# Kernel tuning notes

Hardware: AMD Instinct MI355X
Metric: run time of the kernel (lower is better)

The kernel has to match this reference:

```python
import jax, jax.numpy as jnp
import numpy as np

B, T, OMNI_D, STATIC_D = 128, 1024, 32, 16
H = 64            # hidden // 2 (per-direction GRU size)
HID = 128         # hidden
PHYS_LEN, N_PHYS = 432, 5


def _gelu(x):
    return jax.nn.gelu(x, approximate=False)  # torch GELU default = exact erf


def _ln(x, g, b, eps=1e-5):
    m = jnp.mean(x, -1, keepdims=True)
    v = jnp.var(x, -1, keepdims=True)
    return (x - m) / jnp.sqrt(v + eps) * g + b


def _gru_layer(x, Wih, Whh, bih, bhh, reverse):
    # PyTorch GRU cell math; x: [B,T,D] -> (outputs [B,T,H], h_final [B,H])
    Hh = Whh.shape[1]
    gi = jnp.einsum('btd,gd->btg', x, Wih) + bih  # precompute input projections
    if reverse:
        gi = gi[:, ::-1]
    gi = jnp.swapaxes(gi, 0, 1)  # [T,B,3H]
    h0 = jnp.zeros((x.shape[0], Hh), x.dtype)

    def step(h, g):
        gh = h @ Whh.T + bhh
        r = jax.nn.sigmoid(g[:, :Hh] + gh[:, :Hh])
        z = jax.nn.sigmoid(g[:, Hh:2 * Hh] + gh[:, Hh:2 * Hh])
        n = jnp.tanh(g[:, 2 * Hh:] + r * gh[:, 2 * Hh:])
        hn = (1 - z) * n + z * h
        return hn, hn

    hT, ys = jax.lax.scan(step, h0, gi)
    ys = jnp.swapaxes(ys, 0, 1)
    if reverse:
        ys = ys[:, ::-1]
    return ys, hT


def _conv1d(x, W, b, pad, dil):
    y = jax.lax.conv_general_dilated(x, W, (1,), [(pad, pad)], rhs_dilation=(dil,),
                                     dimension_numbers=('NCH', 'OIH', 'NCH'))
    return y + b[None, :, None]


def setup_inputs():
    key = jax.random.key(0)
    ks = iter(jax.random.split(key, 64))

    def rn(shape, s=0.05):
        return jax.random.normal(next(ks), shape, jnp.float32) * s

    inp = {
        'omni_seq': rn((B, T, OMNI_D), 1.0),
        'static_x': rn((B, STATIC_D), 1.0),
        'phys': rn((B, N_PHYS, PHYS_LEN), 1.0),
    }
    for l, d_in in (('l0', OMNI_D), ('l1', 2 * H)):
        for dr in ('f', 'b'):
            inp[f'gru_Wih_{l}{dr}'] = rn((3 * H, d_in))
            inp[f'gru_Whh_{l}{dr}'] = rn((3 * H, H))
            inp[f'gru_bih_{l}{dr}'] = rn((3 * H,))
            inp[f'gru_bhh_{l}{dr}'] = rn((3 * H,))
    inp['sm_W'] = rn((H, STATIC_D)); inp['sm_b'] = rn((H,))
    inp['sm_ln_g'] = jnp.ones((H,), jnp.float32); inp['sm_ln_b'] = jnp.zeros((H,), jnp.float32)
    inp['gate_W'] = rn((N_PHYS, H)); inp['gate_b'] = rn((N_PHYS,))
    inp['attn_in_W'] = rn((3 * N_PHYS, N_PHYS)); inp['attn_in_b'] = rn((3 * N_PHYS,))
    inp['attn_out_W'] = rn((N_PHYS, N_PHYS)); inp['attn_out_b'] = rn((N_PHYS,))
    for i, ksz in ((1, 3), (2, 5), (3, 9)):
        inp[f'conv{i}_W'] = rn((HID // 4, N_PHYS, ksz)); inp[f'conv{i}_b'] = rn((HID // 4,))
    FUSED = HID + H + 3 * (HID // 4)  # 288
    inp['head_ln_g'] = jnp.ones((FUSED,), jnp.float32); inp['head_ln_b'] = jnp.zeros((FUSED,), jnp.float32)
    inp['head_W1'] = rn((HID, FUSED)); inp['head_b1'] = rn((HID,))
    inp['head_W2'] = rn((PHYS_LEN, HID)); inp['head_b2'] = rn((PHYS_LEN,))
    return inp


def reference(omni_seq, static_x, phys,
              gru_Wih_l0f, gru_Whh_l0f, gru_bih_l0f, gru_bhh_l0f,
              gru_Wih_l0b, gru_Whh_l0b, gru_bih_l0b, gru_bhh_l0b,
              gru_Wih_l1f, gru_Whh_l1f, gru_bih_l1f, gru_bhh_l1f,
              gru_Wih_l1b, gru_Whh_l1b, gru_bih_l1b, gru_bhh_l1b,
              sm_W, sm_b, sm_ln_g, sm_ln_b, gate_W, gate_b,
              attn_in_W, attn_in_b, attn_out_W, attn_out_b,
              conv1_W, conv1_b, conv2_W, conv2_b, conv3_W, conv3_b,
              head_ln_g, head_ln_b, head_W1, head_b1, head_W2, head_b2):
    # --- bidirectional 2-layer GRU (eval mode: dropout off) ---
    y0f, _ = _gru_layer(omni_seq, gru_Wih_l0f, gru_Whh_l0f, gru_bih_l0f, gru_bhh_l0f, False)
    y0b, _ = _gru_layer(omni_seq, gru_Wih_l0b, gru_Whh_l0b, gru_bih_l0b, gru_bhh_l0b, True)
    x1 = jnp.concatenate([y0f, y0b], -1)
    _, hf = _gru_layer(x1, gru_Wih_l1f, gru_Whh_l1f, gru_bih_l1f, gru_bhh_l1f, False)
    _, hb = _gru_layer(x1, gru_Wih_l1b, gru_Whh_l1b, gru_bih_l1b, gru_bhh_l1b, True)
    omni_embed = jnp.concatenate([hf, hb], -1)  # h_omni[-2] ++ h_omni[-1], [B,128]
    # --- static MLP ---
    static_embed = _ln(_gelu(static_x @ sm_W.T + sm_b), sm_ln_g, sm_ln_b)  # [B,64]
    # --- gating on phys channels ---
    gates = jax.nn.sigmoid(static_embed @ gate_W.T + gate_b)[..., None]  # [B,5,1]
    p = phys * gates  # [B,5,432]
    # --- tiny MHA: embed_dim=5, 5 heads, head_dim=1 -> scale = 1/sqrt(1) = 1 ---
    pt = jnp.swapaxes(p, 1, 2)  # [B,432,5]
    qkv = pt @ attn_in_W.T + attn_in_b
    E = N_PHYS
    q, k, v = qkv[..., :E], qkv[..., E:2 * E], qkv[..., 2 * E:]
    scores = jnp.einsum('bih,bjh->bhij', q, k)  # [B,5,432,432]
    attn = jax.nn.softmax(scores, -1)
    ao = jnp.einsum('bhij,bjh->bih', attn, v)
    ao = ao @ attn_out_W.T + attn_out_b  # out_proj
    p = jnp.swapaxes(ao, 1, 2)  # [B,5,432]
    # --- dilated conv branches + GELU + adaptive avg pool (= mean over length) ---
    c1 = _gelu(_conv1d(p, conv1_W, conv1_b, 1, 1)).mean(-1)
    c2 = _gelu(_conv1d(p, conv2_W, conv2_b, 2, 2)).mean(-1)
    c3 = _gelu(_conv1d(p, conv3_W, conv3_b, 4, 4)).mean(-1)
    fused = jnp.concatenate([omni_embed, static_embed, c1, c2, c3], 1)  # [B,288]
    h = _ln(fused, head_ln_g, head_ln_b)
    h = _gelu(h @ head_W1.T + head_b1)  # dropout off in eval
    return h @ head_W2.T + head_b2  # [B,432]
```

## Files before the change

### kernel.cpp

```cpp
#include <hip/hip_runtime.h>
#include <stdint.h>

#define B_ 128
#define T_ 1024
#define BT_ (B_*T_)
#define H_ 64
#define G_ 192
#define PL_ 432
#define NP_ 5
#define FUSED_ 288
#define N_IN 41

typedef unsigned short u16;
typedef __attribute__((ext_vector_type(8))) short bf16x8;
typedef __attribute__((ext_vector_type(4))) float f32x4;
typedef _Float16 h2 __attribute__((ext_vector_type(2)));
typedef _Float16 h8 __attribute__((ext_vector_type(8)));

__device__ inline float bf2f(u16 u){ union{float f; unsigned int i;} c; c.i = ((unsigned int)u)<<16; return c.f; }
__device__ inline u16 f2bf(float f){ unsigned int u = __float_as_uint(f); unsigned int r = (u + 0x7fffu + ((u>>16)&1u))>>16; return (u16)r; }
__device__ inline _Float16 bf2h(u16 u){ return (_Float16)bf2f(u); }
__device__ inline float sigm(float x){ return 1.f/(1.f+__expf(-x)); }
__device__ inline float tanh_(float x){ float t = __expf(fminf(fmaxf(2.f*x,-30.f),30.f)); return (t-1.f)/(t+1.f); }
__device__ inline float gelu_(float x){ return 0.5f*x*(1.f + erff(x*0.70710678118654752f)); }
__device__ inline float wredsum(float v){
  #pragma unroll
  for(int o=32;o>0;o>>=1) v += __shfl_xor(v,o);
  return v;
}

#if __has_builtin(__builtin_amdgcn_fdot2)
__device__ inline float dot2(h2 a, h2 b, float c){ return __builtin_amdgcn_fdot2(a, b, c, false); }
#else
__device__ inline float dot2(h2 a, h2 b, float c){ return c + (float)a.x*(float)b.x + (float)a.y*(float)b.y; }
#endif

struct CvtArgs {
  const void* src[N_IN];
  unsigned dstOff[N_IN];
  unsigned cnt[N_IN];
  unsigned blkStart[N_IN+1];
};

__global__ __launch_bounds__(256) void convert_k(CvtArgs a, u16* __restrict__ dst){
  const bool isbf = (((const u16*)a.src[21])[0] == 0x3F80u);
  int b = blockIdx.x;
  int lo = 0, hi = N_IN;
  while (hi - lo > 1){ int mid = (lo+hi)>>1; if (a.blkStart[mid] <= (unsigned)b) lo = mid; else hi = mid; }
  const int i = lo;
  const unsigned lb = (unsigned)b - a.blkStart[i];
  const unsigned n = a.cnt[i];
  u16* d = dst + a.dstOff[i];
  if (isbf){
    const u16* s = (const u16*)a.src[i];
    #pragma unroll
    for(int e=0;e<8;e++){ unsigned idx = lb*2048u + e*256u + threadIdx.x; if (idx < n) d[idx] = s[idx]; }
  } else {
    const float* s = (const float*)a.src[i];
    #pragma unroll
    for(int e=0;e<8;e++){ unsigned idx = lb*2048u + e*256u + threadIdx.x; if (idx < n) d[idx] = f2bf(s[idx]); }
  }
}

template<int K>
__global__ __launch_bounds__(256) void gi_gemm(const u16* __restrict__ A,
    const u16* __restrict__ Wf, const u16* __restrict__ Wb,
    const u16* __restrict__ biasF, const u16* __restrict__ biasB,
    u16* __restrict__ out)
{
  const int wv = threadIdx.x >> 6, lane = threadIdx.x & 63;
  const int l15 = lane & 15, quad = lane >> 4;
  const size_t mBase = (size_t)blockIdx.x*64 + wv*16;

  bf16x8 afr[K/32];
  #pragma unroll
  for(int kc=0;kc<K/32;kc++)
    afr[kc] = *(const bf16x8*)(A + (mBase + l15)*K + kc*32 + quad*8);

  #pragma unroll
  for(int half=0; half<2; ++half){
    const u16* W    = half ? Wb : Wf;
    const u16* bias = half ? biasB : biasF;
    u16* o = out + (size_t)half * BT_ * G_;
    for(int nt=0; nt<12; ++nt){
      int n = nt*16 + l15;
      f32x4 acc = {0.f,0.f,0.f,0.f};
      #pragma unroll
      for(int kc=0;kc<K/32;kc++){
        bf16x8 bfr = *(const bf16x8*)(W + n*K + kc*32 + quad*8);
        acc = __builtin_amdgcn_mfma_f32_16x16x32_bf16(afr[kc], bfr, acc, 0,0,0);
      }
      float bv = bf2f(bias[n]);
      #pragma unroll
      for(int r=0;r<4;r++){
        size_t row = mBase + quad*4 + r;
        o[row*G_ + n] = f2bf(acc[r] + bv);
      }
    }
  }
}

__global__ __launch_bounds__(64)
void recur(const u16* __restrict__ gi,
    const u16* __restrict__ WhF, const u16* __restrict__ WhB,
    const u16* __restrict__ bhF, const u16* __restrict__ bhB,
    u16* __restrict__ y_x1, float* __restrict__ hfin, int layer)
{
  const int chain = blockIdx.x;
  const int dir = chain >> 7;
  const int b = chain & 127;
  const int j = threadIdx.x;
  const u16* Wh = dir ? WhB : WhF;
  const u16* bh = dir ? bhB : bhF;

  h2 wr[32], wz[32], wn[32];
  #pragma unroll
  for(int k8=0;k8<8;k8++){
    uint4 q;
    q = *(const uint4*)(Wh + (size_t)j*64 + k8*8);
    wr[4*k8+0] = (h2){bf2h((u16)(q.x&0xffffu)), bf2h((u16)(q.x>>16))};
    wr[4*k8+1] = (h2){bf2h((u16)(q.y&0xffffu)), bf2h((u16)(q.y>>16))};
    wr[4*k8+2] = (h2){bf2h((u16)(q.z&0xffffu)), bf2h((u16)(q.z>>16))};
    wr[4*k8+3] = (h2){bf2h((u16)(q.w&0xffffu)), bf2h((u16)(q.w>>16))};
    q = *(const uint4*)(Wh + (size_t)(64+j)*64 + k8*8);
    wz[4*k8+0] = (h2){bf2h((u16)(q.x&0xffffu)), bf2h((u16)(q.x>>16))};
    wz[4*k8+1] = (h2){bf2h((u16)(q.y&0xffffu)), bf2h((u16)(q.y>>16))};
    wz[4*k8+2] = (h2){bf2h((u16)(q.z&0xffffu)), bf2h((u16)(q.z>>16))};
    wz[4*k8+3] = (h2){bf2h((u16)(q.w&0xffffu)), bf2h((u16)(q.w>>16))};
    q = *(const uint4*)(Wh + (size_t)(128+j)*64 + k8*8);
    wn[4*k8+0] = (h2){bf2h((u16)(q.x&0xffffu)), bf2h((u16)(q.x>>16))};
    wn[4*k8+1] = (h2){bf2h((u16)(q.y&0xffffu)), bf2h((u16)(q.y>>16))};
    wn[4*k8+2] = (h2){bf2h((u16)(q.z&0xffffu)), bf2h((u16)(q.z>>16))};
    wn[4*k8+3] = (h2){bf2h((u16)(q.w&0xffffu)), bf2h((u16)(q.w>>16))};
  }
  const float bhr = bf2f(bh[j]), bhz = bf2f(bh[64+j]), bhn = bf2f(bh[128+j]);

  __shared__ __align__(16) u16 giLds[2][3072];
  __shared__ _Float16 hSf[64];
  h8* hS8 = (h8*)hSf;
  hSf[j] = (_Float16)0.f;

  const u16* giC = gi + (size_t)chain * T_ * G_;

  auto issue_chunk = [&](int c, int buf){
    int tbase = dir ? (1008 - c*16) : (c*16);
    const u16* src = giC + (size_t)tbase*G_ + j*8;
    u16* dst = &giLds[buf][0];
    #pragma unroll
    for(int i=0;i<6;i++){
      __builtin_amdgcn_global_load_lds(
        (const __attribute__((address_space(1))) void*)(src + i*512),
        (__attribute__((address_space(3))) void*)(dst + i*512), 16, 0, 0);
    }
  };

  issue_chunk(0, 0);

  float h = 0.f;
  for(int c=0; c<64; ++c){
    asm volatile("s_waitcnt vmcnt(0)" ::: "memory");
    if (c < 63) issue_chunk(c+1, (c+1)&1);
    const u16* gbuf = &giLds[c&1][0];
    #pragma unroll 2
    for(int ls=0; ls<16; ++ls){
      int row = dir ? (15-ls) : ls;
      const u16* rowp = gbuf + row*G_;
      float r0=bhr, r1=0.f, z0=bhz, z1=0.f, n0=bhn, n1=0.f;
      #pragma unroll
      for(int k=0;k<8;k++){
        h8 hv = hS8[k];
        h2 p0 = __builtin_shufflevector(hv, hv, 0, 1);
        h2 p1 = __builtin_shufflevector(hv, hv, 2, 3);
        h2 p2 = __builtin_shufflevector(hv, hv, 4, 5);
        h2 p3 = __builtin_shufflevector(hv, hv, 6, 7);
        r0 = dot2(wr[4*k+0], p0, r0); r1 = dot2(wr[4*k+1], p1, r1);
        r0 = dot2(wr[4*k+2], p2, r0); r1 = dot2(wr[4*k+3], p3, r1);
        z0 = dot2(wz[4*k+0], p0, z0); z1 = dot2(wz[4*k+1], p1, z1);
        z0 = dot2(wz[4*k+2], p2, z0); z1 = dot2(wz[4*k+3], p3, z1);
        n0 = dot2(wn[4*k+0], p0, n0); n1 = dot2(wn[4*k+1], p1, n1);
        n0 = dot2(wn[4*k+2], p2, n0); n1 = dot2(wn[4*k+3], p3, n1);
      }
      float gr = bf2f(rowp[j]), gz = bf2f(rowp[64+j]), gn = bf2f(rowp[128+j]);

      float r  = sigm(gr + (r0+r1));
      float z  = sigm(gz + (z0+z1));
      float nn = tanh_(gn + r*(n0+n1));
      h = (1.f - z)*nn + z*h;

      hSf[j] = (_Float16)h;

      if (layer == 0){
        int s = c*16 + ls;
        int t = dir ? (T_-1-s) : s;
        y_x1[((size_t)b*T_ + t)*128 + dir*64 + j] = f2bf(h);
      }
    }
  }
  if (layer == 1) hfin[b*FUSED_ + dir*64 + j] = h;
}

__global__ __launch_bounds__(64) void static_k(const u16* __restrict__ sx,
   const u16* __restrict__ smW, const u16* __restrict__ smb,
   const u16* __restrict__ lng, const u16* __restrict__ lnb,
   const u16* __restrict__ gW, const u16* __restrict__ gb,
   float* __restrict__ fused, float* __restrict__ gates)
{
  int b = blockIdx.x, j = threadIdx.x;
  float xr[16];
  #pragma unroll
  for(int k=0;k<16;k++) xr[k] = bf2f(sx[b*16+k]);
  float acc = bf2f(smb[j]);
  #pragma unroll
  for(int k=0;k<16;k++) acc += xr[k]*bf2f(smW[j*16+k]);
  float xg = gelu_(acc);
  float m = wredsum(xg)*(1.f/64.f);
  float d = xg - m;
  float v = wredsum(d*d)*(1.f/64.f);
  float se = d*rsqrtf(v+1e-5f)*bf2f(lng[j]) + bf2f(lnb[j]);
  fused[b*FUSED_ + 128 + j] = se;
  #pragma unroll
  for(int i=0;i<5;i++){
    float p = se*bf2f(gW[i*64+j]);
    float s = wredsum(p);
    if (j == 0) gates[b*5+i] = sigm(s + bf2f(gb[i]));
  }
}

__global__ __launch_bounds__(448) void qkv_k(const u16* __restrict__ phys,
   const float* __restrict__ gates, const u16* __restrict__ aW,
   const u16* __restrict__ ab, float* __restrict__ qkv)
{
  int b = blockIdx.x, l = threadIdx.x;
  if (l >= PL_) return;
  float pv[5];
  #pragma unroll
  for(int i=0;i<5;i++) pv[i] = bf2f(phys[((size_t)b*5+i)*PL_ + l]) * gates[b*5+i];
  #pragma unroll
  for(int c=0;c<15;c++){
    float a = bf2f(ab[c]);
    #pragma unroll
    for(int i=0;i<5;i++) a += pv[i]*bf2f(aW[c*5+i]);
    qkv[((size_t)b*15+c)*PL_ + l] = a;
  }
}

__global__ __launch_bounds__(256) void attn_k(const float* __restrict__ qkv,
                                              float* __restrict__ ao)
{
  int h = blockIdx.x, b = blockIdx.y;
  int tid = threadIdx.x;
  __shared__ float kS[PL_], vS[PL_];
  __shared__ float red[32];
  const float* qb = qkv + ((size_t)b*15 + h)*PL_;
  const float* kb = qkv + ((size_t)b*15 + 5 + h)*PL_;
  const float* vb = qkv + ((size_t)b*15 + 10 + h)*PL_;
  for(int j=tid;j<PL_;j+=256){ kS[j]=kb[j]; vS[j]=vb[j]; }
  __syncthreads();
  float lmax=-1e30f, lmin=1e30f;
  for(int j=tid;j<PL_;j+=256){ float kv=kS[j]; lmax=fmaxf(lmax,kv); lmin=fminf(lmin,kv); }
  #pragma unroll
  for(int o=32;o>0;o>>=1){ lmax=fmaxf(lmax,__shfl_xor(lmax,o)); lmin=fminf(lmin,__shfl_xor(lmin,o)); }
  int wv = tid>>6;
  if ((tid&63)==0){ red[wv]=lmax; red[8+wv]=lmin; }
  __syncthreads();
  if (tid==0){
    float mx=red[0], mn=red[8];
    for(int i=1;i<4;i++){ mx=fmaxf(mx,red[i]); mn=fminf(mn,red[8+i]); }
    red[16]=mx; red[17]=mn;
  }
  __syncthreads();
  float kmx=red[16], kmn=red[17];
  for(int i=tid;i<PL_;i+=256){
    float s = qb[i];
    float m = fmaxf(s*kmx, s*kmn);
    float den=0.f, num=0.f;
    #pragma unroll 4
    for(int j=0;j<PL_;j++){
      float e = __expf(s*kS[j]-m);
      den += e; num += e*vS[j];
    }
    ao[((size_t)b*PL_+i)*5 + h] = num/den;
  }
}

__global__ __launch_bounds__(448) void proj_k(const float* __restrict__ ao,
   const u16* __restrict__ oW, const u16* __restrict__ ob, float* __restrict__ p2)
{
  int b = blockIdx.x, l = threadIdx.x;
  if (l >= PL_) return;
  float a[5];
  #pragma unroll
  for(int hh=0;hh<5;hh++) a[hh] = ao[((size_t)b*PL_+l)*5 + hh];
  #pragma unroll
  for(int c=0;c<5;c++){
    float s = bf2f(ob[c]);
    #pragma unroll
    for(int hh=0;hh<5;hh++) s += a[hh]*bf2f(oW[c*5+hh]);
    p2[((size_t)b*5+c)*PL_ + l] = s;
  }
}

template<int KS, int DIL, int PAD>
__device__ inline void do_conv(const float* pS, const u16* Wc, const u16* bc,
                               float* fused, int b, int o, int p, int cslot)
{
  const int Lout = PL_ + 2*PAD - DIL*(KS-1);
  float w[5][KS];
  #pragma unroll
  for(int i=0;i<5;i++)
    #pragma unroll
    for(int t=0;t<KS;t++) w[i][t] = bf2f(Wc[(o*5+i)*KS + t]);
  float bias = bf2f(bc[o]);
  float acc = 0.f;
  for(int l=p; l<Lout; l+=8){
    float s = bias;
    #pragma unroll
    for(int t=0;t<KS;t++){
      int idx = l - PAD + t*DIL;
      if (idx >= 0 && idx < PL_){
        #pragma unroll
        for(int i=0;i<5;i++) s += w[i][t]*pS[i*PL_ + idx];
      }
    }
    acc += gelu_(s);
  }
  #pragma unroll
  for(int off=1;off<8;off<<=1) acc += __shfl_xor(acc,off);
  if (p == 0) fused[b*FUSED_ + 192 + cslot*32 + o] = acc/(float)Lout;
}

__global__ __launch_bounds__(256) void conv_k(const float* __restrict__ p2,
  const u16* __restrict__ W1c, const u16* __restrict__ b1c,
  const u16* __restrict__ W2c, const u16* __restrict__ b2c,
  const u16* __restrict__ W3c, const u16* __restrict__ b3c,
  float* __restrict__ fused)
{
  int b = blockIdx.x;
  __shared__ float pS[5*PL_];
  for(int idx=threadIdx.x; idx<5*PL_; idx+=256) pS[idx] = p2[(size_t)b*5*PL_ + idx];
  __syncthreads();
  int o = threadIdx.x >> 3, p = threadIdx.x & 7;
  do_conv<3,1,1>(pS, W1c, b1c, fused, b, o, p, 0);
  do_conv<5,2,2>(pS, W2c, b2c, fused, b, o, p, 1);
  do_conv<9,4,4>(pS, W3c, b3c, fused, b, o, p, 2);
}

__global__ __launch_bounds__(448) void head_k(const float* __restrict__ fused,
   const u16* __restrict__ lng, const u16* __restrict__ lnb,
   const u16* __restrict__ W1, const u16* __restrict__ b1,
   const u16* __restrict__ W2, const u16* __restrict__ b2,
   void* __restrict__ out, const u16* __restrict__ detect)
{
  const bool isbf = (detect[0] == 0x3F80u);
  int b = blockIdx.x, tid = threadIdx.x;
  __shared__ float fS[FUSED_];
  __shared__ float hS[128];
  __shared__ float red[32];
  float v = (tid < FUSED_) ? fused[b*FUSED_ + tid] : 0.f;
  float s1 = wredsum(v);
  float s2 = wredsum(v*v);
  int wv = tid>>6;
  if ((tid&63)==0){ red[wv]=s1; red[8+wv]=s2; }
  __syncthreads();
  if (tid==0){
    float S=0.f, SS=0.f;
    for(int i=0;i<7;i++){ S+=red[i]; SS+=red[8+i]; }
    float m = S/288.f;
    red[16]=m; red[17]=SS/288.f - m*m;
  }
  __syncthreads();
  float m = red[16], var = red[17];
  if (tid < FUSED_) fS[tid] = (v-m)*rsqrtf(var+1e-5f)*bf2f(lng[tid]) + bf2f(lnb[tid]);
  __syncthreads();
  if (tid < 128){
    float a = bf2f(b1[tid]);
    const u16* wr = W1 + (size_t)tid*FUSED_;
    #pragma unroll
    for(int k8=0;k8<36;k8++){
      uint4 q = *(const uint4*)(wr + k8*8);
      a += fS[8*k8+0]*bf2f((u16)(q.x&0xffffu)) + fS[8*k8+1]*bf2f((u16)(q.x>>16))
         + fS[8*k8+2]*bf2f((u16)(q.y&0xffffu)) + fS[8*k8+3]*bf2f((u16)(q.y>>16))
         + fS[8*k8+4]*bf2f((u16)(q.z&0xffffu)) + fS[8*k8+5]*bf2f((u16)(q.z>>16))
         + fS[8*k8+6]*bf2f((u16)(q.w&0xffffu)) + fS[8*k8+7]*bf2f((u16)(q.w>>16));
    }
    hS[tid] = gelu_(a);
  }
  __syncthreads();
  if (tid < PL_){
    float a = bf2f(b2[tid]);
    const u16* wr = W2 + (size_t)tid*128;
    #pragma unroll
    for(int k8=0;k8<16;k8++){
      uint4 q = *(const uint4*)(wr + k8*8);
      a += hS[8*k8+0]*bf2f((u16)(q.x&0xffffu)) + hS[8*k8+1]*bf2f((u16)(q.x>>16))
         + hS[8*k8+2]*bf2f((u16)(q.y&0xffffu)) + hS[8*k8+3]*bf2f((u16)(q.y>>16))
         + hS[8*k8+4]*bf2f((u16)(q.z&0xffffu)) + hS[8*k8+5]*bf2f((u16)(q.z>>16))
         + hS[8*k8+6]*bf2f((u16)(q.w&0xffffu)) + hS[8*k8+7]*bf2f((u16)(q.w>>16));
    }
    size_t oi = (size_t)b*PL_ + tid;
    if (isbf) ((u16*)out)[oi] = f2bf(a);
    else      ((float*)out)[oi] = a;
  }
}

extern "C" void kernel_launch(void* const* d_in, const int* in_sizes, int n_in,
                              void* d_out, int out_size, void* d_ws, size_t ws_size,
                              hipStream_t stream)
{
  static const unsigned cnts[N_IN] = {
    4194304, 2048, 276480,
    6144, 12288, 192, 192,
    6144, 12288, 192, 192,
    24576, 12288, 192, 192,
    24576, 12288, 192, 192,
    1024, 64, 64, 64,
    320, 5,
    75, 15,
    25, 5,
    480, 32, 800, 32, 1440, 32,
    288, 288,
    36864, 128, 55296, 432
  };

  char* ws = (char*)d_ws;
  size_t off = 0;
  auto alloc = [&](size_t bytes){ size_t o = off; off = (off + bytes + 255) & ~(size_t)255; return o; };

  CvtArgs ca;
  const u16* cin[N_IN];
  unsigned totalBlocks = 0;
  for (int i=0;i<N_IN;i++){
    ca.src[i] = d_in[i];
    ca.cnt[i] = cnts[i];
    size_t o = alloc((size_t)cnts[i]*2);
    ca.dstOff[i] = (unsigned)(o/2);
    cin[i] = (const u16*)(ws + o);
    ca.blkStart[i] = totalBlocks;
    totalBlocks += (cnts[i] + 2047u)/2048u;
  }
  ca.blkStart[N_IN] = totalBlocks;
  u16* canon = (u16*)ws;

  u16*   gi    = (u16*)  (ws + alloc((size_t)2*BT_*G_*2));
  u16*   x1    = (u16*)  (ws + alloc((size_t)BT_*128*2));
  float* fused = (float*)(ws + alloc((size_t)B_*FUSED_*4));
  float* gates = (float*)(ws + alloc((size_t)B_*5*4));
  float* qkv   = (float*)(ws + alloc((size_t)B_*15*PL_*4));
  float* ao    = (float*)(ws + alloc((size_t)B_*PL_*5*4));
  float* p2    = (float*)(ws + alloc((size_t)B_*5*PL_*4));
  (void)ws_size; (void)in_sizes; (void)n_in; (void)out_size;

  convert_k<<<totalBlocks, 256, 0, stream>>>(ca, canon);

  gi_gemm<32><<<BT_/64, 256, 0, stream>>>(cin[0], cin[3], cin[7], cin[5], cin[9], gi);
  recur<<<256, 64, 0, stream>>>(gi, cin[4], cin[8], cin[6], cin[10], x1, nullptr, 0);
  gi_gemm<128><<<BT_/64, 256, 0, stream>>>(x1, cin[11], cin[15], cin[13], cin[17], gi);
  recur<<<256, 64, 0, stream>>>(gi, cin[12], cin[16], cin[14], cin[18], nullptr, fused, 1);
  static_k<<<128, 64, 0, stream>>>(cin[1], cin[19], cin[20], cin[21], cin[22], cin[23], cin[24], fused, gates);
  qkv_k<<<128, 448, 0, stream>>>(cin[2], gates, cin[25], cin[26], qkv);
  attn_k<<<dim3(5,128), 256, 0, stream>>>(qkv, ao);
  proj_k<<<128, 448, 0, stream>>>(ao, cin[27], cin[28], p2);
  conv_k<<<128, 256, 0, stream>>>(p2, cin[29], cin[30], cin[31], cin[32], cin[33], cin[34], fused);
  head_k<<<128, 448, 0, stream>>>(fused, cin[35], cin[36], cin[37], cin[38], cin[39], cin[40],
                                  d_out, (const u16*)d_in[21]);
}
```

Before: 1.288 ms.

## Split GRU recurrence gates across three waves with a dedicated loader wave

The recurrence kernel grows from one wave to four per chain. Three waves each compute one gate's hidden-state dot products, exchanging pre-activations through LDS with a workgroup barrier every timestep. The fourth wave prefetches gi chunks and writes the layer-0 outputs back from an LDS history buffer. This cuts the serial dot-product length per step to a third and moves global stores off the critical path. In exchange, every step now pays an s_barrier plus an extra LDS round trip, and the h-state LDS update may race with the next step's reads without a second barrier.

```diff
diff --git a/kernel.cpp b/kernel.cpp
--- a/kernel.cpp
+++ b/kernel.cpp
@@ -27,6 +27,9 @@
   #pragma unroll
   for(int o=32;o>0;o>>=1) v += __shfl_xor(v,o);
   return v;
+}
+__device__ inline void wg_barrier(){
+  asm volatile("s_waitcnt lgkmcnt(0)\n\ts_barrier" ::: "memory");
 }
 
 #if __has_builtin(__builtin_amdgcn_fdot2)
@@ -100,7 +103,7 @@
   }
 }
 
-__global__ __launch_bounds__(64)
+__global__ __launch_bounds__(256)
 void recur(const u16* __restrict__ gi,
     const u16* __restrict__ WhF, const u16* __restrict__ WhB,
     const u16* __restrict__ bhF, const u16* __restrict__ bhB,
@@ -109,43 +112,37 @@
   const int chain = blockIdx.x;
   const int dir = chain >> 7;
   const int b = chain & 127;
-  const int j = threadIdx.x;
+  const int tid = threadIdx.x;
+  const int j = tid & 63;
   const u16* Wh = dir ? WhB : WhF;
   const u16* bh = dir ? bhB : bhF;
 
-  h2 wr[32], wz[32], wn[32];
-  #pragma unroll
-  for(int k8=0;k8<8;k8++){
-    uint4 q;
-    q = *(const uint4*)(Wh + (size_t)j*64 + k8*8);
-    wr[4*k8+0] = (h2){bf2h((u16)(q.x&0xffffu)), bf2h((u16)(q.x>>16))};
-    wr[4*k8+1] = (h2){bf2h((u16)(q.y&0xffffu)), bf2h((u16)(q.y>>16))};
-    wr[4*k8+2] = (h2){bf2h((u16)(q.z&0xffffu)), bf2h((u16)(q.z>>16))};
-    wr[4*k8+3] = (h2){bf2h((u16)(q.w&0xffffu)), bf2h((u16)(q.w>>16))};
-    q = *(const uint4*)(Wh + (size_t)(64+j)*64 + k8*8);
-    wz[4*k8+0] = (h2){bf2h((u16)(q.x&0xffffu)), bf2h((u16)(q.x>>16))};
-    wz[4*k8+1] = (h2){bf2h((u16)(q.y&0xffffu)), bf2h((u16)(q.y>>16))};
-    wz[4*k8+2] = (h2){bf2h((u16)(q.z&0xffffu)), bf2h((u16)(q.z>>16))};
-    wz[4*k8+3] = (h2){bf2h((u16)(q.w&0xffffu)), bf2h((u16)(q.w>>16))};
-    q = *(const uint4*)(Wh + (size_t)(128+j)*64 + k8*8);
-    wn[4*k8+0] = (h2){bf2h((u16)(q.x&0xffffu)), bf2h((u16)(q.x>>16))};
-    wn[4*k8+1] = (h2){bf2h((u16)(q.y&0xffffu)), bf2h((u16)(q.y>>16))};
-    wn[4*k8+2] = (h2){bf2h((u16)(q.z&0xffffu)), bf2h((u16)(q.z>>16))};
-    wn[4*k8+3] = (h2){bf2h((u16)(q.w&0xffffu)), bf2h((u16)(q.w>>16))};
-  }
-  const float bhr = bf2f(bh[j]), bhz = bf2f(bh[64+j]), bhn = bf2f(bh[128+j]);
-
-  __shared__ __align__(16) u16 giLds[2][3072];
-  __shared__ _Float16 hSf[64];
-  h8* hS8 = (h8*)hSf;
-  hSf[j] = (_Float16)0.f;
+  __shared__ __align__(16) u16 giL[2][16*G_];
+  __shared__ float preS[2][192];
+  __shared__ __align__(16) _Float16 hS[64];
+  __shared__ u16 hHist[2][16][64];
+  h8* hS8 = (h8*)hS;
+
+  h2 w[32];
+  float bias = 0.f;
+  if (tid < 192){
+    #pragma unroll
+    for(int k8=0;k8<8;k8++){
+      uint4 q = *(const uint4*)(Wh + (size_t)tid*64 + k8*8);
+      w[4*k8+0] = (h2){bf2h((u16)(q.x&0xffffu)), bf2h((u16)(q.x>>16))};
+      w[4*k8+1] = (h2){bf2h((u16)(q.y&0xffffu)), bf2h((u16)(q.y>>16))};
+      w[4*k8+2] = (h2){bf2h((u16)(q.z&0xffffu)), bf2h((u16)(q.z>>16))};
+      w[4*k8+3] = (h2){bf2h((u16)(q.w&0xffffu)), bf2h((u16)(q.w>>16))};
+    }
+    bias = bf2f(bh[tid]);
+  }
 
   const u16* giC = gi + (size_t)chain * T_ * G_;
 
   auto issue_chunk = [&](int c, int buf){
     int tbase = dir ? (1008 - c*16) : (c*16);
     const u16* src = giC + (size_t)tbase*G_ + j*8;
-    u16* dst = &giLds[buf][0];
+    u16* dst = &giL[buf][0];
     #pragma unroll
     for(int i=0;i<6;i++){
       __builtin_amdgcn_global_load_lds(
@@ -154,18 +151,21 @@
     }
   };
 
-  issue_chunk(0, 0);
+  if (tid < 64) hS[tid] = (_Float16)0.f;
+  if (tid >= 192){
+    issue_chunk(0, 0);
+    asm volatile("s_waitcnt vmcnt(0)" ::: "memory");
+  }
+  wg_barrier();
 
   float h = 0.f;
-  for(int c=0; c<64; ++c){
-    asm volatile("s_waitcnt vmcnt(0)" ::: "memory");
-    if (c < 63) issue_chunk(c+1, (c+1)&1);
-    const u16* gbuf = &giLds[c&1][0];
-    #pragma unroll 2
-    for(int ls=0; ls<16; ++ls){
-      int row = dir ? (15-ls) : ls;
-      const u16* rowp = gbuf + row*G_;
-      float r0=bhr, r1=0.f, z0=bhz, z1=0.f, n0=bhn, n1=0.f;
+  for(int s=0; s<T_; ++s){
+    const int c = s >> 4, ls = s & 15, p = s & 1;
+    const int rls = dir ? (15 - ls) : ls;
+    const u16* gbuf = &giL[c & 1][0];
+
+    if (tid < 192){
+      float a0 = 0.f, a1 = 0.f, a2 = 0.f, a3 = 0.f;
       #pragma unroll
       for(int k=0;k<8;k++){
         h8 hv = hS8[k];
@@ -173,30 +173,58 @@
         h2 p1 = __builtin_shufflevector(hv, hv, 2, 3);
         h2 p2 = __builtin_shufflevector(hv, hv, 4, 5);
         h2 p3 = __builtin_shufflevector(hv, hv, 6, 7);
-        r0 = dot2(wr[4*k+0], p0, r0); r1 = dot2(wr[4*k+1], p1, r1);
-        r0 = dot2(wr[4*k+2], p2, r0); r1 = dot2(wr[4*k+3], p3, r1);
-        z0 = dot2(wz[4*k+0], p0, z0); z1 = dot2(wz[4*k+1], p1, z1);
-        z0 = dot2(wz[4*k+2], p2, z0); z1 = dot2(wz[4*k+3], p3, z1);
-        n0 = dot2(wn[4*k+0], p0, n0); n1 = dot2(wn[4*k+1], p1, n1);
-        n0 = dot2(wn[4*k+2], p2, n0); n1 = dot2(wn[4*k+3], p3, n1);
+        a0 = dot2(w[4*k+0], p0, a0);
+        a1 = dot2(w[4*k+1], p1, a1);
+        a2 = dot2(w[4*k+2], p2, a2);
+        a3 = dot2(w[4*k+3], p3, a3);
       }
-      float gr = bf2f(rowp[j]), gz = bf2f(rowp[64+j]), gn = bf2f(rowp[128+j]);
-
-      float r  = sigm(gr + (r0+r1));
-      float z  = sigm(gz + (z0+z1));
-      float nn = tanh_(gn + r*(n0+n1));
+      float acc = bias + (a0+a1)+(a2+a3);
+      if (tid < 128) acc += bf2f(gbuf[rls*G_ + tid]);
+      preS[p][tid] = acc;
+    } else {
+      if (ls == 15) asm volatile("s_waitcnt vmcnt(0)" ::: "memory");
+    }
+
+    wg_barrier();
+
+    if (tid < 192){
+      float pr = preS[p][j];
+      float pz = preS[p][64+j];
+      float pn = preS[p][128+j];
+      float gn = bf2f(gbuf[rls*G_ + 128 + j]);
+      float r  = sigm(pr);
+      float z  = sigm(pz);
+      float nn = tanh_(gn + r*pn);
       h = (1.f - z)*nn + z*h;
-
-      hSf[j] = (_Float16)h;
-
-      if (layer == 0){
-        int s = c*16 + ls;
-        int t = dir ? (T_-1-s) : s;
-        y_x1[((size_t)b*T_ + t)*128 + dir*64 + j] = f2bf(h);
+      hS[j] = (_Float16)h;
+      if (tid < 64) hHist[c&1][ls][j] = f2bf(h);
+    } else {
+      if (ls == 0){
+        int cn = c + 1;
+        if (cn < 64) issue_chunk(cn, cn & 1);
+        if (layer == 0 && c > 0){
+          int cc = c - 1;
+          #pragma unroll 4
+          for(int l2=0;l2<16;l2++){
+            int s2 = cc*16 + l2;
+            int t = dir ? (T_-1-s2) : s2;
+            y_x1[((size_t)b*T_ + t)*128 + dir*64 + j] = hHist[cc&1][l2][j];
+          }
+        }
       }
     }
   }
-  if (layer == 1) hfin[b*FUSED_ + dir*64 + j] = h;
+
+  wg_barrier();
+  if (tid >= 192 && layer == 0){
+    #pragma unroll 4
+    for(int l2=0;l2<16;l2++){
+      int s2 = 63*16 + l2;
+      int t = dir ? (T_-1-s2) : s2;
+      y_x1[((size_t)b*T_ + t)*128 + dir*64 + j] = hHist[1][l2][j];
+    }
+  }
+  if (layer == 1 && tid < 64) hfin[b*FUSED_ + dir*64 + tid] = h;
 }
 
 __global__ __launch_bounds__(64) void static_k(const u16* __restrict__ sx,
@@ -453,9 +481,9 @@
   convert_k<<<totalBlocks, 256, 0, stream>>>(ca, canon);
 
   gi_gemm<32><<<BT_/64, 256, 0, stream>>>(cin[0], cin[3], cin[7], cin[5], cin[9], gi);
-  recur<<<256, 64, 0, stream>>>(gi, cin[4], cin[8], cin[6], cin[10], x1, nullptr, 0);
+  recur<<<256, 256, 0, stream>>>(gi, cin[4], cin[8], cin[6], cin[10], x1, nullptr, 0);
   gi_gemm<128><<<BT_/64, 256, 0, stream>>>(x1, cin[11], cin[15], cin[13], cin[17], gi);
-  recur<<<256, 64, 0, stream>>>(gi, cin[12], cin[16], cin[14], cin[18], nullptr, fused, 1);
+  recur<<<256, 256, 0, stream>>>(gi, cin[12], cin[16], cin[14], cin[18], nullptr, fused, 1);
   static_k<<<128, 64, 0, stream>>>(cin[1], cin[19], cin[20], cin[21], cin[22], cin[23], cin[24], fused, gates);
   qkv_k<<<128, 448, 0, stream>>>(cin[2], gates, cin[25], cin[26], qkv);
   attn_k<<<dim3(5,128), 256, 0, stream>>>(qkv, ao);
```

Result: slower. 1.482 ms (+15.0%).
